# Optimization experiments

Measured on AMD Instinct MI355X. Metric: run time of the kernel, lower is better.

Reference implementation:

```python
import jax, jax.numpy as jnp
import numpy as np

N_NODES = 100000
D = 128


def gcn_conv(x, W, b, src, dst, deg_inv_sqrt):
    # PyG GCNConv: linear transform, symmetric-normalized aggregation with self-loops, bias
    h = x @ W  # [N, D_out]
    norm = deg_inv_sqrt[src] * deg_inv_sqrt[dst]  # [E_tot]
    msgs = h[src] * norm[:, None]  # gather + scale  [E_tot, D_out]
    out = jax.ops.segment_sum(msgs, dst, num_segments=x.shape[0])  # scatter-add to targets
    return out + b


def _prep_edges(edge_index, n_nodes):
    # add self-loops (weight 1) and compute deg^{-1/2} over targets (flow source_to_target)
    loops = jnp.arange(n_nodes, dtype=edge_index.dtype)
    src = jnp.concatenate([edge_index[0], loops])
    dst = jnp.concatenate([edge_index[1], loops])
    deg = jax.ops.segment_sum(jnp.ones_like(dst, dtype=jnp.float32), dst, num_segments=n_nodes)
    deg_inv_sqrt = jnp.where(deg > 0, jax.lax.rsqrt(jnp.maximum(deg, 1.0)), 0.0)
    return src, dst, deg_inv_sqrt


def setup_inputs() -> dict:
    key = jax.random.key(0)
    ks = jax.random.split(key, 8)
    node_fts = jax.random.normal(ks[0], (N_NODES, D), dtype=jnp.float32)
    edge_index = jax.random.randint(ks[1], (2, 1600000), 0, N_NODES, dtype=jnp.int64)
    scale = 1.0 / np.sqrt(D)
    W1 = jax.random.uniform(ks[2], (D, D), jnp.float32, -scale, scale)
    b1 = jnp.zeros((D,), jnp.float32)
    W2 = jax.random.uniform(ks[3], (D, D), jnp.float32, -scale, scale)
    b2 = jnp.zeros((D,), jnp.float32)
    W3 = jax.random.uniform(ks[4], (D, D), jnp.float32, -scale, scale)
    b3 = jnp.zeros((D,), jnp.float32)
    return {"node_fts": node_fts, "edge_index": edge_index,
            "W1": W1, "b1": b1, "W2": W2, "b2": b2, "W3": W3, "b3": b3}


def reference(node_fts, edge_index, W1, b1, W2, b2, W3, b3):
    n = node_fts.shape[0]
    src, dst, dinv = _prep_edges(edge_index, n)
    x = jax.nn.relu(gcn_conv(node_fts, W1, b1, src, dst, dinv))
    x = jax.nn.relu(gcn_conv(x, W2, b2, src, dst, dinv))
    x = jax.nn.relu(gcn_conv(x, W3, b3, src, dst, dinv))
    return x
```

## Files before the change

kernel.cpp:

```cpp
#include <hip/hip_runtime.h>

#define NN 100000
#define EE 1600000
#define D 128
#define NPART 8
#define PSZ (NN / NPART)
#define NI4 (EE / 4)
#define SUBW 196
#define NSB (NPART * 64)
#define SCAP 4096
#define RCAP 8192
#define LBCAP 96

typedef __attribute__((ext_vector_type(8))) short bf16x8;
typedef __attribute__((ext_vector_type(4))) float f32x4;

__device__ inline unsigned int f2bf2(float a, float b) {
    unsigned int ua = __float_as_uint(a);
    unsigned int ub = __float_as_uint(b);
    ua = (ua + 0x7fffu + ((ua >> 16) & 1u)) >> 16;
    ub = (ub + 0x7fffu + ((ub >> 16) & 1u)) >> 16;
    return ua | (ub << 16);
}
__device__ inline unsigned short f2bf(float a) {
    unsigned int u = __float_as_uint(a);
    return (unsigned short)((u + 0x7fffu + ((u >> 16) & 1u)) >> 16);
}
__device__ inline float2 bf2f2(unsigned int u) {
    return make_float2(__uint_as_float(u << 16), __uint_as_float(u & 0xffff0000u));
}


__global__ void init_kernel(int* __restrict__ gcur2, unsigned int* __restrict__ xsA,
                            unsigned int* __restrict__ xsB) {
    int i = blockIdx.x * blockDim.x + threadIdx.x;
    if (i < NSB) gcur2[i] = 0;
    if (i < 64) {
        xsA[(size_t)NN * 64 + i] = 0;
        xsB[(size_t)NN * 64 + i] = 0;
    }
}

__global__ __launch_bounds__(256) void filterbin_kernel(const int4* __restrict__ src4,
                                                        const int4* __restrict__ dst4,
                                                        int* __restrict__ gcur2,
                                                        uint2* __restrict__ buckets2) {
    __shared__ uint2 bins[64][LBCAP];
    __shared__ int bcnt[64];
    __shared__ int gbase[64];
    const int p = blockIdx.x >> 6;
    const int c = blockIdx.x & 63;
    if (threadIdx.x < 64) bcnt[threadIdx.x] = 0;
    __syncthreads();
    const int lo = p * PSZ, hi = lo + PSZ;
    const int chunk4 = NI4 / 64;
    const int a0 = c * chunk4, a1 = a0 + chunk4;
    for (int i = a0 + threadIdx.x; i < a1; i += 256) {
        int4 d4 = dst4[i];
        bool m0 = (d4.x >= lo && d4.x < hi);
        bool m1 = (d4.y >= lo && d4.y < hi);
        bool m2 = (d4.z >= lo && d4.z < hi);
        bool m3 = (d4.w >= lo && d4.w < hi);
        if (!(m0 | m1 | m2 | m3)) continue;
        int4 s4 = src4[i];
        int ss[4] = {s4.x, s4.y, s4.z, s4.w};
        int dd[4] = {d4.x, d4.y, d4.z, d4.w};
        bool mm[4] = {m0, m1, m2, m3};
#pragma unroll
        for (int k = 0; k < 4; ++k) {
            if (!mm[k]) continue;
            int li = (dd[k] - lo) / SUBW;
            int pos = atomicAdd(&bcnt[li], 1);
            if (pos < LBCAP) {
                bins[li][pos] = make_uint2((unsigned)ss[k], (unsigned)dd[k]);
            } else {
                int sb = p * 64 + li;
                int gp = atomicAdd(&gcur2[sb], 1);
                buckets2[(size_t)sb * SCAP + gp] = make_uint2((unsigned)ss[k], (unsigned)dd[k]);
            }
        }
    }
    __syncthreads();
    if (threadIdx.x < 64) {
        int cc = min(bcnt[threadIdx.x], LBCAP);
        gbase[threadIdx.x] = atomicAdd(&gcur2[p * 64 + threadIdx.x], cc);
        bcnt[threadIdx.x] = cc;
    }
    __syncthreads();
    for (int b = 0; b < 64; ++b) {
        const int cc = bcnt[b];
        uint2* outp = buckets2 + (size_t)(p * 64 + b) * SCAP + gbase[b];
        for (int i = threadIdx.x; i < cc; i += 256) outp[i] = bins[b][i];
    }
}

__global__ __launch_bounds__(256) void sort3_kernel(const uint2* __restrict__ buckets2,
                                                    const int* __restrict__ gcur2,
                                                    int* __restrict__ csr,
                                                    int* __restrict__ info,
                                                    float* __restrict__ dinv) {
    __shared__ int hist[256];
    __shared__ int pscan[256];
    __shared__ int lcur[256];
    __shared__ int staged[RCAP];
    const int sb = blockIdx.x;
    const int li = sb & 63;
    const int base_node = (sb >> 6) * PSZ + li * SUBW;
    const int nnodes = min(SUBW, PSZ - li * SUBW);
    const int scnt = gcur2[sb];
    const uint2* bk = buckets2 + (size_t)sb * SCAP;
    const int t = threadIdx.x;
    hist[t] = 0;
    __syncthreads();
    for (int i = t; i < scnt; i += 256) atomicAdd(&hist[(int)bk[i].y - base_node], 1);
    __syncthreads();
    const int padded = (t < nnodes) ? ((hist[t] + 7) & ~7) : 0;
    pscan[t] = padded;
    __syncthreads();
    for (int off = 1; off < 256; off <<= 1) {
        int v = (t >= off) ? pscan[t - off] : 0;
        __syncthreads();
        pscan[t] += v;
        __syncthreads();
    }
    const int rstart = pscan[t] - padded;
    lcur[t] = rstart;
    __syncthreads();
    const int total = pscan[255];
    for (int i = t; i < total; i += 256) staged[i] = NN;
    __syncthreads();
    for (int i = t; i < scnt; i += 256) {
        uint2 r = bk[i];
        int pos = atomicAdd(&lcur[(int)r.y - base_node], 1);
        staged[pos] = (int)r.x;
    }
    __syncthreads();
    int4* co = (int4*)(csr + (size_t)sb * RCAP);
    for (int i = t; i < (total >> 2); i += 256) co[i] = ((const int4*)staged)[i];
    if (t < nnodes) {
        int dg = hist[t];
        info[base_node + t] = ((sb * RCAP + rstart) << 8) | dg;
        dinv[base_node + t] = rsqrtf(1.0f + (float)dg);
    }
}

__global__ void wt_build3_kernel(const float* __restrict__ W1, const float* __restrict__ W2,
                                 const float* __restrict__ W3, unsigned short* __restrict__ wt1,
                                 unsigned short* __restrict__ wt2, unsigned short* __restrict__ wt3) {
    const int which = blockIdx.x >> 6;
    const float* W = which == 0 ? W1 : (which == 1 ? W2 : W3);
    unsigned short* wt = which == 0 ? wt1 : (which == 1 ? wt2 : wt3);
    int i = (blockIdx.x & 63) * 256 + threadIdx.x;
    int n = i >> 7, k = i & 127;
    wt[n * 128 + k] = f2bf(W[k * 128 + n]);
}

__global__ __launch_bounds__(256) void scale0_kernel(const float* __restrict__ x0,
                                                     const float* __restrict__ dinv,
                                                     unsigned int* __restrict__ xs) {
    int i = blockIdx.x * 256 + threadIdx.x;
    int row = i >> 5, c = (i & 31) * 4;
    float4 v = *(const float4*)(x0 + (size_t)row * 128 + c);
    float dv = dinv[row];
    *(uint2*)(xs + (size_t)row * 64 + (c >> 1)) =
        make_uint2(f2bf2(v.x * dv, v.y * dv), f2bf2(v.z * dv, v.w * dv));
}


template <bool LAST>
__global__ __launch_bounds__(256) void fused_kernel(const unsigned int* __restrict__ xs,
                                                    const unsigned short* __restrict__ wt,
                                                    const int* __restrict__ csr,
                                                    const int* __restrict__ info,
                                                    const float* __restrict__ dinv,
                                                    const float* __restrict__ bias,
                                                    void* __restrict__ outp) {
    __shared__ unsigned int ylds[64 * 68];
    const int w = threadIdx.x >> 6;
    const int j = threadIdx.x & 63;
    const int base = blockIdx.x * 64;

    for (int i = 0; i < 16; ++i) {
        const int d = base + w * 16 + i;
        if (d >= NN) break;
        const int ifo = info[d];
        int e = ifo >> 8;
        const int end = e + (((ifo & 255) + 7) & ~7);
        float2 acc = bf2f2(xs[(size_t)d * 64 + j]);
        for (; e + 16 <= end; e += 16) {
            int4 c0 = *(const int4*)(csr + e);
            int4 c1 = *(const int4*)(csr + e + 4);
            int4 c2 = *(const int4*)(csr + e + 8);
            int4 c3 = *(const int4*)(csr + e + 12);
            unsigned int v0 = xs[(size_t)c0.x * 64 + j];
            unsigned int v1 = xs[(size_t)c0.y * 64 + j];
            unsigned int v2 = xs[(size_t)c0.z * 64 + j];
            unsigned int v3 = xs[(size_t)c0.w * 64 + j];
            unsigned int v4 = xs[(size_t)c1.x * 64 + j];
            unsigned int v5 = xs[(size_t)c1.y * 64 + j];
            unsigned int v6 = xs[(size_t)c1.z * 64 + j];
            unsigned int v7 = xs[(size_t)c1.w * 64 + j];
            unsigned int v8 = xs[(size_t)c2.x * 64 + j];
            unsigned int v9 = xs[(size_t)c2.y * 64 + j];
            unsigned int va = xs[(size_t)c2.z * 64 + j];
            unsigned int vb = xs[(size_t)c2.w * 64 + j];
            unsigned int vc = xs[(size_t)c3.x * 64 + j];
            unsigned int vd = xs[(size_t)c3.y * 64 + j];
            unsigned int ve = xs[(size_t)c3.z * 64 + j];
            unsigned int vf = xs[(size_t)c3.w * 64 + j];
            float2 f0 = bf2f2(v0), f1 = bf2f2(v1), f2 = bf2f2(v2), f3 = bf2f2(v3);
            float2 f4 = bf2f2(v4), f5 = bf2f2(v5), f6 = bf2f2(v6), f7 = bf2f2(v7);
            float2 f8 = bf2f2(v8), f9 = bf2f2(v9), fa = bf2f2(va), fb = bf2f2(vb);
            float2 fc = bf2f2(vc), fd = bf2f2(vd), fe = bf2f2(ve), ff = bf2f2(vf);
            acc.x += ((f0.x + f1.x) + (f2.x + f3.x)) + ((f4.x + f5.x) + (f6.x + f7.x)) +
                     ((f8.x + f9.x) + (fa.x + fb.x)) + ((fc.x + fd.x) + (fe.x + ff.x));
            acc.y += ((f0.y + f1.y) + (f2.y + f3.y)) + ((f4.y + f5.y) + (f6.y + f7.y)) +
                     ((f8.y + f9.y) + (fa.y + fb.y)) + ((fc.y + fd.y) + (fe.y + ff.y));
        }
        if (e < end) {
            int4 c0 = *(const int4*)(csr + e);
            int4 c1 = *(const int4*)(csr + e + 4);
            unsigned int v0 = xs[(size_t)c0.x * 64 + j];
            unsigned int v1 = xs[(size_t)c0.y * 64 + j];
            unsigned int v2 = xs[(size_t)c0.z * 64 + j];
            unsigned int v3 = xs[(size_t)c0.w * 64 + j];
            unsigned int v4 = xs[(size_t)c1.x * 64 + j];
            unsigned int v5 = xs[(size_t)c1.y * 64 + j];
            unsigned int v6 = xs[(size_t)c1.z * 64 + j];
            unsigned int v7 = xs[(size_t)c1.w * 64 + j];
            float2 f0 = bf2f2(v0), f1 = bf2f2(v1), f2 = bf2f2(v2), f3 = bf2f2(v3);
            float2 f4 = bf2f2(v4), f5 = bf2f2(v5), f6 = bf2f2(v6), f7 = bf2f2(v7);
            acc.x += ((f0.x + f1.x) + (f2.x + f3.x)) + ((f4.x + f5.x) + (f6.x + f7.x));
            acc.y += ((f0.y + f1.y) + (f2.y + f3.y)) + ((f4.y + f5.y) + (f6.y + f7.y));
        }
        const float dv = dinv[d];
        ylds[(w * 16 + i) * 68 + j] = f2bf2(dv * acc.x, dv * acc.y);
    }
    __syncthreads();

    const int r = j & 15;
    const int q = j >> 4;
    const unsigned short* wrow = wt + (size_t)r * 128 + q * 8;
    const int myrow = w * 16 + r;
    f32x4 acc[8] = {};
#pragma unroll
    for (int kc = 0; kc < 4; ++kc) {
        bf16x8 xf = *(const bf16x8*)(ylds + myrow * 68 + q * 4 + kc * 16);
#pragma unroll
        for (int nt = 0; nt < 8; ++nt) {
            bf16x8 wf = *(const bf16x8*)(wrow + (size_t)nt * 16 * 128 + kc * 32);
            acc[nt] = __builtin_amdgcn_mfma_f32_16x16x32_bf16(wf, xf, acc[nt], 0, 0, 0);
        }
    }
    const int orow = base + myrow;
    if (orow >= NN) return;
    if (LAST) {
        float* op = (float*)outp + (size_t)orow * 128;
#pragma unroll
        for (int nt = 0; nt < 8; ++nt) {
            int n = nt * 16 + q * 4;
            float4 bb = *(const float4*)(bias + n);
            float4 o;
            o.x = fmaxf(acc[nt][0] + bb.x, 0.0f);
            o.y = fmaxf(acc[nt][1] + bb.y, 0.0f);
            o.z = fmaxf(acc[nt][2] + bb.z, 0.0f);
            o.w = fmaxf(acc[nt][3] + bb.w, 0.0f);
            *(float4*)(op + n) = o;
        }
    } else {
        const float dvr = dinv[orow];
        unsigned int* op = (unsigned int*)outp + (size_t)orow * 64;
#pragma unroll
        for (int nt = 0; nt < 8; ++nt) {
            int n = nt * 16 + q * 4;
            float4 bb = *(const float4*)(bias + n);
            float o0 = fmaxf(acc[nt][0] + bb.x, 0.0f) * dvr;
            float o1 = fmaxf(acc[nt][1] + bb.y, 0.0f) * dvr;
            float o2 = fmaxf(acc[nt][2] + bb.z, 0.0f) * dvr;
            float o3 = fmaxf(acc[nt][3] + bb.w, 0.0f) * dvr;
            *(uint2*)(op + (n >> 1)) = make_uint2(f2bf2(o0, o1), f2bf2(o2, o3));
        }
    }
}


extern "C" void kernel_launch(void* const* d_in, const int* in_sizes, int n_in,
                              void* d_out, int out_size, void* d_ws, size_t ws_size,
                              hipStream_t stream) {
    const float* x0 = (const float*)d_in[0];
    const int* ei = (const int*)d_in[1];
    const float* W1 = (const float*)d_in[2];
    const float* b1 = (const float*)d_in[3];
    const float* W2 = (const float*)d_in[4];
    const float* b2 = (const float*)d_in[5];
    const float* W3 = (const float*)d_in[6];
    const float* b3 = (const float*)d_in[7];
    float* out = (float*)d_out;

    char* ws = (char*)d_ws;
    size_t off = 0;
    auto alloc = [&](size_t bytes) -> void* {
        off = (off + 511) & ~(size_t)511;
        void* p = ws + off;
        off += bytes;
        return p;
    };
    unsigned int* xsA = (unsigned int*)alloc(((size_t)NN + 1) * 64 * 4);
    int*   csr     = (int*)  alloc((size_t)NSB * RCAP * sizeof(int));
    uint2* buckets2 = (uint2*)alloc((size_t)NSB * SCAP * sizeof(uint2));
    int*   info    = (int*)  alloc((size_t)NN * sizeof(int));
    float* dinv    = (float*)alloc((size_t)NN * sizeof(float));
    int*   gcur2   = (int*)  alloc(NSB * sizeof(int));
    unsigned short* wt1 = (unsigned short*)alloc(128 * 128 * 2);
    unsigned short* wt2 = (unsigned short*)alloc(128 * 128 * 2);
    unsigned short* wt3 = (unsigned short*)alloc(128 * 128 * 2);

    unsigned int* xsB = (unsigned int*)d_out;

    const int4* src4 = (const int4*)ei;
    const int4* dst4 = (const int4*)(ei + EE);

    init_kernel<<<2, 256, 0, stream>>>(gcur2, xsA, xsB);
    filterbin_kernel<<<NSB, 256, 0, stream>>>(src4, dst4, gcur2, buckets2);
    sort3_kernel<<<NSB, 256, 0, stream>>>(buckets2, gcur2, csr, info, dinv);
    wt_build3_kernel<<<192, 256, 0, stream>>>(W1, W2, W3, wt1, wt2, wt3);
    scale0_kernel<<<NN * 32 / 256, 256, 0, stream>>>(x0, dinv, xsA);

    const int fusedBlocks = (NN + 63) / 64;

    fused_kernel<false><<<fusedBlocks, 256, 0, stream>>>(xsA, wt1, csr, info, dinv, b1, (void*)xsB);
    fused_kernel<false><<<fusedBlocks, 256, 0, stream>>>(xsB, wt2, csr, info, dinv, b2, (void*)xsA);
    fused_kernel<true><<<fusedBlocks, 256, 0, stream>>>(xsA, wt3, csr, info, dinv, b3, (void*)out);
}
```

Before: 462.2 us.

## Shrink fused GCN blocks to 16 rows for more parallelism

Each fused block now aggregates 16 destination rows (4 per wave) instead of 64, so the grid has four times as many blocks and each wave's serial gather loop is shorter. The MFMA transform still runs on 16-row tiles, but each 16-row tile now repeats 4 real rows, so three quarters of the matrix work is redundant and only lanes with r<4 write output. The goal is better latency hiding and load balance for the memory-bound gather, at the cost of wasted MFMA work, reloading the weight fragments in every block, and more block launches. NN/16 divides exactly, so the bounds checks were removed.

```diff
diff --git a/kernel.cpp b/kernel.cpp
--- a/kernel.cpp
+++ b/kernel.cpp
@@ -175,14 +175,14 @@
                                                     const float* __restrict__ dinv,
                                                     const float* __restrict__ bias,
                                                     void* __restrict__ outp) {
-    __shared__ unsigned int ylds[64 * 68];
+    __shared__ unsigned int ylds[16 * 68];
     const int w = threadIdx.x >> 6;
     const int j = threadIdx.x & 63;
-    const int base = blockIdx.x * 64;
-
-    for (int i = 0; i < 16; ++i) {
-        const int d = base + w * 16 + i;
-        if (d >= NN) break;
+    const int rbase = blockIdx.x * 16 + w * 4;
+
+#pragma unroll
+    for (int i = 0; i < 4; ++i) {
+        const int d = rbase + i;
         const int ifo = info[d];
         int e = ifo >> 8;
         const int end = e + (((ifo & 255) + 7) & ~7);
@@ -234,26 +234,26 @@
             acc.y += ((f0.y + f1.y) + (f2.y + f3.y)) + ((f4.y + f5.y) + (f6.y + f7.y));
         }
         const float dv = dinv[d];
-        ylds[(w * 16 + i) * 68 + j] = f2bf2(dv * acc.x, dv * acc.y);
+        ylds[(w * 4 + i) * 68 + j] = f2bf2(dv * acc.x, dv * acc.y);
     }
     __syncthreads();
 
     const int r = j & 15;
     const int q = j >> 4;
     const unsigned short* wrow = wt + (size_t)r * 128 + q * 8;
-    const int myrow = w * 16 + r;
-    f32x4 acc[8] = {};
+    const int lrow = w * 4 + (r & 3);
+    f32x4 acc2[8] = {};
 #pragma unroll
     for (int kc = 0; kc < 4; ++kc) {
-        bf16x8 xf = *(const bf16x8*)(ylds + myrow * 68 + q * 4 + kc * 16);
+        bf16x8 xf = *(const bf16x8*)(ylds + lrow * 68 + q * 4 + kc * 16);
 #pragma unroll
         for (int nt = 0; nt < 8; ++nt) {
             bf16x8 wf = *(const bf16x8*)(wrow + (size_t)nt * 16 * 128 + kc * 32);
-            acc[nt] = __builtin_amdgcn_mfma_f32_16x16x32_bf16(wf, xf, acc[nt], 0, 0, 0);
-        }
-    }
-    const int orow = base + myrow;
-    if (orow >= NN) return;
+            acc2[nt] = __builtin_amdgcn_mfma_f32_16x16x32_bf16(wf, xf, acc2[nt], 0, 0, 0);
+        }
+    }
+    if (r >= 4) return;
+    const int orow = rbase + r;
     if (LAST) {
         float* op = (float*)outp + (size_t)orow * 128;
 #pragma unroll
@@ -261,10 +261,10 @@
             int n = nt * 16 + q * 4;
             float4 bb = *(const float4*)(bias + n);
             float4 o;
-            o.x = fmaxf(acc[nt][0] + bb.x, 0.0f);
-            o.y = fmaxf(acc[nt][1] + bb.y, 0.0f);
-            o.z = fmaxf(acc[nt][2] + bb.z, 0.0f);
-            o.w = fmaxf(acc[nt][3] + bb.w, 0.0f);
+            o.x = fmaxf(acc2[nt][0] + bb.x, 0.0f);
+            o.y = fmaxf(acc2[nt][1] + bb.y, 0.0f);
+            o.z = fmaxf(acc2[nt][2] + bb.z, 0.0f);
+            o.w = fmaxf(acc2[nt][3] + bb.w, 0.0f);
             *(float4*)(op + n) = o;
         }
     } else {
@@ -274,10 +274,10 @@
         for (int nt = 0; nt < 8; ++nt) {
             int n = nt * 16 + q * 4;
             float4 bb = *(const float4*)(bias + n);
-            float o0 = fmaxf(acc[nt][0] + bb.x, 0.0f) * dvr;
-            float o1 = fmaxf(acc[nt][1] + bb.y, 0.0f) * dvr;
-            float o2 = fmaxf(acc[nt][2] + bb.z, 0.0f) * dvr;
-            float o3 = fmaxf(acc[nt][3] + bb.w, 0.0f) * dvr;
+            float o0 = fmaxf(acc2[nt][0] + bb.x, 0.0f) * dvr;
+            float o1 = fmaxf(acc2[nt][1] + bb.y, 0.0f) * dvr;
+            float o2 = fmaxf(acc2[nt][2] + bb.z, 0.0f) * dvr;
+            float o3 = fmaxf(acc2[nt][3] + bb.w, 0.0f) * dvr;
             *(uint2*)(op + (n >> 1)) = make_uint2(f2bf2(o0, o1), f2bf2(o2, o3));
         }
     }
@@ -326,7 +326,7 @@
     wt_build3_kernel<<<192, 256, 0, stream>>>(W1, W2, W3, wt1, wt2, wt3);
     scale0_kernel<<<NN * 32 / 256, 256, 0, stream>>>(x0, dinv, xsA);
 
-    const int fusedBlocks = (NN + 63) / 64;
+    const int fusedBlocks = NN / 16;
 
     fused_kernel<false><<<fusedBlocks, 256, 0, stream>>>(xsA, wt1, csr, info, dinv, b1, (void*)xsB);
     fused_kernel<false><<<fusedBlocks, 256, 0, stream>>>(xsB, wt2, csr, info, dinv, b2, (void*)xsA);
```

After: 612.7 us. 1.33x slower.
